# Performance work log

Hardware: AMD Instinct MI355X
Metric: run time of the kernel (lower is better)

## Reference

```python
import jax, jax.numpy as jnp
import numpy as np

NUM_LEVELS = 16
F_PER_LEVEL = 2
LOG2_T = 19
TABLE_SIZE = 1 << LOG2_T  # 524288 entries per level
BASE_RES = 16
DESIRED_RES = 4096
PER_LEVEL_SCALE = np.exp(np.log(DESIRED_RES / BASE_RES) / (NUM_LEVELS - 1))
PRIMES = (np.uint32(1), np.uint32(2654435761), np.uint32(805459861))
N_POINTS = 4_194_304

# 8 corner offsets of the trilinear cell, bit i of corner index -> dim offset
_CORNERS = jnp.array([[(i >> d) & 1 for d in range(3)] for i in range(8)], dtype=jnp.float32)  # [8,3]


def hashgrid_encode(texc, table):
    """texc: [N,3] in [0,1]; table: [L, T, F]. Returns [N, L*F] (tcnn HashGrid math)."""
    feats = []
    for lvl in range(NUM_LEVELS):
        scale = float(np.exp2(lvl * np.log2(PER_LEVEL_SCALE)) * BASE_RES - 1.0)
        res = int(np.ceil(scale)) + 1
        pos = texc * scale + 0.5                    # [N,3]
        pg = jnp.floor(pos)
        frac = pos - pg                             # [N,3]
        corner = pg[:, None, :] + _CORNERS[None]    # [N,8,3]
        ci = corner.astype(jnp.uint32)
        # trilinear weights: prod over dims of frac (offset=1) or 1-frac (offset=0)
        w = jnp.prod(jnp.where(_CORNERS[None] == 1.0, frac[:, None, :], 1.0 - frac[:, None, :]), axis=-1)  # [N,8]
        if res ** 3 <= TABLE_SIZE:
            # dense level: index = x + y*res + z*res^2
            idx = ci[..., 0] + ci[..., 1] * jnp.uint32(res) + ci[..., 2] * jnp.uint32(res * res)
        else:
            # hashed level: spatial hash with xor of per-dim primes, mod 2^19
            idx = (ci[..., 0] * PRIMES[0]) ^ (ci[..., 1] * PRIMES[1]) ^ (ci[..., 2] * PRIMES[2])
            idx = idx & jnp.uint32(TABLE_SIZE - 1)
        g = table[lvl][idx.astype(jnp.int32)]       # [N,8,F] irregular gather
        feats.append(jnp.einsum('nc,ncf->nf', w, g))
    return jnp.concatenate(feats, axis=-1)          # [N, 32]


def setup_inputs() -> dict:
    key = jax.random.key(0)
    k0, k1, k2, k3, k4 = jax.random.split(key, 5)
    texc = jax.random.uniform(k0, (N_POINTS, 3), dtype=jnp.float32)
    # tcnn inits hashgrid params uniform in [-1e-4, 1e-4]
    table = (jax.random.uniform(k1, (NUM_LEVELS, TABLE_SIZE, F_PER_LEVEL), dtype=jnp.float32) * 2.0 - 1.0) * 1e-4
    # kaiming_uniform (relu) bound = sqrt(6/fan_in)
    def kaiming(k, shape):
        bound = float(np.sqrt(6.0 / shape[1]))
        return jax.random.uniform(k, shape, dtype=jnp.float32, minval=-bound, maxval=bound)
    W0 = kaiming(k2, (32, 32))
    W1 = kaiming(k3, (32, 32))
    W2 = kaiming(k4, (3, 32))
    return {"texc": texc, "table": table, "W0": W0, "W1": W1, "W2": W2}


def reference(texc, table, W0, W1, W2):
    enc = hashgrid_encode(texc, table)              # [N,32]
    h = jax.nn.relu(enc @ W0.T)
    h = jax.nn.relu(h @ W1.T)
    out = jax.nn.sigmoid(h @ W2.T)                  # [N,3]
    return out
```

## Files before the change

### kernel.cpp

```cpp
#include <hip/hip_runtime.h>
#include <math.h>

#define NUM_LEVELS 16
#define N_DENSE 5
#define N_HASH (NUM_LEVELS - N_DENSE)
#define TABLE_SIZE (1u << 19)
#define TMASK (TABLE_SIZE - 1u)

typedef float f32x4 __attribute__((ext_vector_type(4)));
typedef float f32x2 __attribute__((ext_vector_type(2)));
typedef short s16x8 __attribute__((ext_vector_type(8)));
typedef unsigned u32x2 __attribute__((ext_vector_type(2)));
typedef unsigned u32x4 __attribute__((ext_vector_type(4)));

struct HashParams { float scale[N_HASH]; };
struct DenseParams { float scale[N_DENSE]; unsigned res[N_DENSE]; };
struct AllParams { float scale[NUM_LEVELS]; unsigned res[NUM_LEVELS]; };

static __device__ __forceinline__ unsigned bf16_bits(float f) {
    const unsigned u = __builtin_bit_cast(unsigned, f);
    return (u + (0x7fffu + ((u >> 16) & 1u))) >> 16;
}
static __device__ __forceinline__ short bf16s(float f) { return (short)bf16_bits(f); }
static __device__ __forceinline__ float bflo(unsigned v) { return __builtin_bit_cast(float, v << 16); }
static __device__ __forceinline__ float bfhi(unsigned v) { return __builtin_bit_cast(float, v & 0xffff0000u); }

static __device__ __forceinline__ s16x8 packW8(const float* __restrict__ p) {
    const f32x4 a = *(const f32x4*)p;
    const f32x4 b = *(const f32x4*)(p + 4);
    s16x8 v;
    v[0] = bf16s(a.x); v[1] = bf16s(a.y); v[2] = bf16s(a.z); v[3] = bf16s(a.w);
    v[4] = bf16s(b.x); v[5] = bf16s(b.y); v[6] = bf16s(b.z); v[7] = bf16s(b.w);
    return v;
}
static __device__ __forceinline__ s16x8 packW8sig(const float* __restrict__ row, int q) {
    const f32x4 lo = *(const f32x4*)(row + 4 * q);
    const f32x4 hi = *(const f32x4*)(row + 16 + 4 * q);
    s16x8 v;
    v[0] = bf16s(lo.x); v[1] = bf16s(hi.x); v[2] = bf16s(lo.y); v[3] = bf16s(hi.y);
    v[4] = bf16s(lo.z); v[5] = bf16s(hi.z); v[6] = bf16s(lo.w); v[7] = bf16s(hi.w);
    return v;
}

__global__ __launch_bounds__(256) void cvt_table_kernel(
    const f32x4* __restrict__ src, u32x2* __restrict__ dst, int n2)
{
    const int i = blockIdx.x * 256 + threadIdx.x;
    if (i >= n2) return;
    const f32x4 g = __builtin_nontemporal_load(src + i);
    u32x2 o;
    o.x = bf16_bits(g.x) | (bf16_bits(g.y) << 16);
    o.y = bf16_bits(g.z) | (bf16_bits(g.w) << 16);
    dst[i] = o;
}

template <bool BT>
__global__ __launch_bounds__(256) void hashed_all_kernel(
    const float* __restrict__ texc,
    const float* __restrict__ tf,
    const unsigned* __restrict__ tb,
    unsigned* __restrict__ enc_ws,
    int n, int B, HashParams P)
{
    __shared__ float tst[768];
    const int tid = threadIdx.x;
    const unsigned lvl = blockIdx.x / (unsigned)B;
    const unsigned blk = blockIdx.x - lvl * (unsigned)B;
    const int i0 = (int)blk * 256;

    tst[tid]       = __builtin_nontemporal_load(texc + 3 * i0 + tid);
    tst[tid + 256] = __builtin_nontemporal_load(texc + 3 * i0 + tid + 256);
    tst[tid + 512] = __builtin_nontemporal_load(texc + 3 * i0 + tid + 512);
    __syncthreads();

    const float s = P.scale[lvl];
    const float tx = tst[3 * tid + 0], ty = tst[3 * tid + 1], tz = tst[3 * tid + 2];

    const float px = tx * s + 0.5f, py = ty * s + 0.5f, pz = tz * s + 0.5f;
    const float gx = floorf(px), gy = floorf(py), gz = floorf(pz);
    const float wx = px - gx, wy = py - gy, wz = pz - gz;
    const unsigned x0 = (unsigned)gx, y0 = (unsigned)gy, z0 = (unsigned)gz;

    const unsigned hy0 = y0 * 2654435761u, hy1 = (y0 + 1u) * 2654435761u;
    const unsigned hz0 = z0 * 805459861u,  hz1 = (z0 + 1u) * 805459861u;
    const unsigned hh[4] = { hy0 ^ hz0, hy1 ^ hz0, hy0 ^ hz1, hy1 ^ hz1 };
    const float wyz[4] = { (1.f - wy) * (1.f - wz), wy * (1.f - wz),
                           (1.f - wy) * wz,         wy * wz };
    const float wx0 = 1.f - wx, wx1 = wx;

    float f0 = 0.f, f1 = 0.f;

    if constexpr (BT) {
        const unsigned* tbl = tb + ((size_t)(N_DENSE + lvl) << 19);
        if ((x0 & 1u) == 0u) {
#pragma unroll
            for (int c = 0; c < 4; ++c) {
                const unsigned idx0 = (x0 ^ hh[c]) & TMASK;
                const u32x2 g = *(const u32x2*)(tbl + (idx0 & ~1u));
                const bool sw = (idx0 & 1u) != 0u;
                const unsigned ea = sw ? g.y : g.x;
                const unsigned eb = sw ? g.x : g.y;
                f0 += wyz[c] * (wx0 * bflo(ea) + wx1 * bflo(eb));
                f1 += wyz[c] * (wx0 * bfhi(ea) + wx1 * bfhi(eb));
            }
        } else {
#pragma unroll
            for (int c = 0; c < 4; ++c) {
                const unsigned ea = tbl[(x0 ^ hh[c]) & TMASK];
                const unsigned eb = tbl[((x0 + 1u) ^ hh[c]) & TMASK];
                f0 += wyz[c] * (wx0 * bflo(ea) + wx1 * bflo(eb));
                f1 += wyz[c] * (wx0 * bfhi(ea) + wx1 * bfhi(eb));
            }
        }
    } else {
        const float* tbl = tf + ((size_t)(N_DENSE + lvl) << 20);
        if ((x0 & 1u) == 0u) {
#pragma unroll
            for (int c = 0; c < 4; ++c) {
                const unsigned idx0 = (x0 ^ hh[c]) & TMASK;
                const f32x4 g = *(const f32x4*)(tbl + 2 * (size_t)(idx0 & ~1u));
                const bool hi = (idx0 & 1u) != 0u;
                const float g0x = hi ? g.z : g.x, g0y = hi ? g.w : g.y;
                const float g1x = hi ? g.x : g.z, g1y = hi ? g.y : g.w;
                f0 += wyz[c] * (wx0 * g0x + wx1 * g1x);
                f1 += wyz[c] * (wx0 * g0y + wx1 * g1y);
            }
        } else {
#pragma unroll
            for (int c = 0; c < 4; ++c) {
                const unsigned ia = (x0 ^ hh[c]) & TMASK;
                const unsigned ib = ((x0 + 1u) ^ hh[c]) & TMASK;
                const f32x2 ga = *(const f32x2*)(tbl + 2 * (size_t)ia);
                const f32x2 gb = *(const f32x2*)(tbl + 2 * (size_t)ib);
                f0 += wyz[c] * (wx0 * ga.x + wx1 * gb.x);
                f1 += wyz[c] * (wx0 * ga.y + wx1 * gb.y);
            }
        }
    }

    const unsigned packed = bf16_bits(f0) | (bf16_bits(f1) << 16);
    __builtin_nontemporal_store(packed, enc_ws + (size_t)lvl * n + (i0 + tid));
}

template <bool BT>
__global__ __launch_bounds__(256) void dense_mlp_kernel(
    const float* __restrict__ texc,
    const float* __restrict__ tf,
    const unsigned* __restrict__ tb,
    const unsigned* __restrict__ enc_ws,
    const float* __restrict__ W0,
    const float* __restrict__ W1,
    const float* __restrict__ W2,
    float* __restrict__ out,
    int n, DenseParams P)
{
    __shared__ float tst[768];
    __shared__ __align__(16) unsigned char slabs[4 * 64 * 80];
    const int tid = threadIdx.x;
    const int i0 = blockIdx.x * 256;

    tst[tid]       = __builtin_nontemporal_load(texc + 3 * i0 + tid);
    tst[tid + 256] = __builtin_nontemporal_load(texc + 3 * i0 + tid + 256);
    tst[tid + 512] = __builtin_nontemporal_load(texc + 3 * i0 + tid + 512);
    __syncthreads();

    const int i = i0 + tid;
    unsigned dd[16];

#pragma unroll
    for (int l = 0; l < N_HASH; ++l)
        dd[N_DENSE + l] = __builtin_nontemporal_load(enc_ws + (size_t)l * n + i);

    const float tx = tst[3 * tid + 0], ty = tst[3 * tid + 1], tz = tst[3 * tid + 2];

#pragma unroll
    for (int l = 0; l < N_DENSE; ++l) {
        const float s = P.scale[l];
        const unsigned res = P.res[l];
        const unsigned res2 = res * res;
        const float px = tx * s + 0.5f, py = ty * s + 0.5f, pz = tz * s + 0.5f;
        const float gx = floorf(px), gy = floorf(py), gz = floorf(pz);
        const float wx = px - gx, wy = py - gy, wz = pz - gz;
        const unsigned x0 = (unsigned)gx, y0 = (unsigned)gy, z0 = (unsigned)gz;
        const float wx0 = 1.f - wx, wx1 = wx;
        const float wyz[4] = { (1.f - wy) * (1.f - wz), wy * (1.f - wz),
                               (1.f - wy) * wz,         wy * wz };
        const unsigned base[4] = { y0 * res + z0 * res2, (y0 + 1u) * res + z0 * res2,
                                   y0 * res + (z0 + 1u) * res2,
                                   (y0 + 1u) * res + (z0 + 1u) * res2 };
        float f0 = 0.f, f1 = 0.f;
        if constexpr (BT) {
            const unsigned* tbl = tb + ((size_t)l << 19);
#pragma unroll
            for (int c = 0; c < 4; ++c) {
                const unsigned idx0 = x0 + base[c];
                unsigned ea, eb;
                if ((idx0 & 1u) == 0u) {
                    const u32x2 g = *(const u32x2*)(tbl + idx0);
                    ea = g.x; eb = g.y;
                } else {
                    ea = tbl[idx0]; eb = tbl[idx0 + 1u];
                }
                f0 += wyz[c] * (wx0 * bflo(ea) + wx1 * bflo(eb));
                f1 += wyz[c] * (wx0 * bfhi(ea) + wx1 * bfhi(eb));
            }
        } else {
            const float* tbl = tf + ((size_t)l << 20);
#pragma unroll
            for (int c = 0; c < 4; ++c) {
                const unsigned idx0 = x0 + base[c];
                if ((idx0 & 1u) == 0u) {
                    const f32x4 g = *(const f32x4*)(tbl + 2 * (size_t)idx0);
                    f0 += wyz[c] * (wx0 * g.x + wx1 * g.z);
                    f1 += wyz[c] * (wx0 * g.y + wx1 * g.w);
                } else {
                    const f32x2 ga = *(const f32x2*)(tbl + 2 * (size_t)idx0);
                    const f32x2 gb = *(const f32x2*)(tbl + 2 * (size_t)(idx0 + 1u));
                    f0 += wyz[c] * (wx0 * ga.x + wx1 * gb.x);
                    f1 += wyz[c] * (wx0 * ga.y + wx1 * gb.y);
                }
            }
        }
        dd[l] = bf16_bits(f0) | (bf16_bits(f1) << 16);
    }

    const int lane = tid & 63;
    const int wv = tid >> 6;
    const int c16 = lane & 15, q = lane >> 4;
    unsigned char* slabB = slabs + wv * (64 * 80);
    unsigned* slab = (unsigned*)slabB;

    *(u32x4*)(slabB + lane * 80 +  0) = (u32x4){ dd[0],  dd[1],  dd[2],  dd[3]  };
    *(u32x4*)(slabB + lane * 80 + 16) = (u32x4){ dd[4],  dd[5],  dd[6],  dd[7]  };
    *(u32x4*)(slabB + lane * 80 + 32) = (u32x4){ dd[8],  dd[9],  dd[10], dd[11] };
    *(u32x4*)(slabB + lane * 80 + 48) = (u32x4){ dd[12], dd[13], dd[14], dd[15] };

    const s16x8 b00 = packW8(W0 + c16 * 32 + 8 * q);
    const s16x8 b01 = packW8(W0 + (16 + c16) * 32 + 8 * q);
    const s16x8 b10 = packW8sig(W1 + c16 * 32, q);
    const s16x8 b11 = packW8sig(W1 + (16 + c16) * 32, q);
    const f32x4 zero4 = { 0.f, 0.f, 0.f, 0.f };

    f32x4 d0[4][2];
#pragma unroll
    for (int t = 0; t < 4; ++t) {
        const s16x8 a = *(const s16x8*)(slabB + (16 * t + c16) * 80 + 16 * q);
        d0[t][0] = __builtin_amdgcn_mfma_f32_16x16x32_bf16(a, b00, zero4, 0, 0, 0);
        d0[t][1] = __builtin_amdgcn_mfma_f32_16x16x32_bf16(a, b01, zero4, 0, 0, 0);
    }
#pragma unroll
    for (int t = 0; t < 4; ++t)
#pragma unroll
        for (int r = 0; r < 4; ++r) {
            const unsigned pk = bf16_bits(fmaxf(d0[t][0][r], 0.f)) |
                                (bf16_bits(fmaxf(d0[t][1][r], 0.f)) << 16);
            slab[(16 * t + 4 * q + r) * 20 + c16] = pk;
        }

    f32x4 d1[4][2];
#pragma unroll
    for (int t = 0; t < 4; ++t) {
        const s16x8 a = *(const s16x8*)(slabB + (16 * t + c16) * 80 + 16 * q);
        d1[t][0] = __builtin_amdgcn_mfma_f32_16x16x32_bf16(a, b10, zero4, 0, 0, 0);
        d1[t][1] = __builtin_amdgcn_mfma_f32_16x16x32_bf16(a, b11, zero4, 0, 0, 0);
    }
#pragma unroll
    for (int t = 0; t < 4; ++t)
#pragma unroll
        for (int r = 0; r < 4; ++r) {
            const unsigned pk = bf16_bits(fmaxf(d1[t][0][r], 0.f)) |
                                (bf16_bits(fmaxf(d1[t][1][r], 0.f)) << 16);
            slab[(16 * t + 4 * q + r) * 20 + c16] = pk;
        }

    float z0 = 0.f, z1 = 0.f, z2 = 0.f;
#pragma unroll
    for (int d = 0; d < 16; ++d) {
        const unsigned v = slab[lane * 20 + d];
        const float a0 = bflo(v), a1 = bfhi(v);
        z0 = fmaf(a0, W2[0 * 32 + d], fmaf(a1, W2[0 * 32 + 16 + d], z0));
        z1 = fmaf(a0, W2[1 * 32 + d], fmaf(a1, W2[1 * 32 + 16 + d], z1));
        z2 = fmaf(a0, W2[2 * 32 + d], fmaf(a1, W2[2 * 32 + 16 + d], z2));
    }
    out[3 * i + 0] = 1.f / (1.f + __expf(-z0));
    out[3 * i + 1] = 1.f / (1.f + __expf(-z1));
    out[3 * i + 2] = 1.f / (1.f + __expf(-z2));
}

__global__ __launch_bounds__(256) void mono_kernel(
    const float* __restrict__ texc, const float* __restrict__ table,
    const float* __restrict__ W0, const float* __restrict__ W1,
    const float* __restrict__ W2, float* __restrict__ out, int n, AllParams p)
{
    int i = blockIdx.x * 256 + threadIdx.x;
    if (i >= n) return;
    const float tx = texc[3 * i], ty = texc[3 * i + 1], tz = texc[3 * i + 2];
    float enc[2 * NUM_LEVELS];
#pragma unroll
    for (int l = 0; l < NUM_LEVELS; ++l) {
        const float s = p.scale[l];
        const unsigned res = p.res[l];
        const float px = tx * s + 0.5f, py = ty * s + 0.5f, pz = tz * s + 0.5f;
        const float gx = floorf(px), gy = floorf(py), gz = floorf(pz);
        const float wx = px - gx, wy = py - gy, wz = pz - gz;
        const unsigned x0 = (unsigned)gx, y0 = (unsigned)gy, z0 = (unsigned)gz;
        const float2* tbl = (const float2*)(table + ((size_t)l << 20));
        float f0 = 0.f, f1 = 0.f;
#pragma unroll
        for (int c = 0; c < 8; ++c) {
            const unsigned dx = c & 1u, dy = (c >> 1) & 1u, dz = (c >> 2) & 1u;
            const unsigned xi = x0 + dx, yi = y0 + dy, zi = z0 + dz;
            unsigned idx;
            if (l < N_DENSE) idx = xi + yi * res + zi * res * res;
            else idx = (xi ^ (yi * 2654435761u) ^ (zi * 805459861u)) & TMASK;
            const float2 g = tbl[idx];
            const float w = (dx ? wx : 1.f - wx) * (dy ? wy : 1.f - wy) *
                            (dz ? wz : 1.f - wz);
            f0 = fmaf(w, g.x, f0);
            f1 = fmaf(w, g.y, f1);
        }
        enc[2 * l] = f0;
        enc[2 * l + 1] = f1;
    }
    float h1[32];
#pragma unroll
    for (int j = 0; j < 32; ++j) {
        float acc = 0.f;
#pragma unroll
        for (int k = 0; k < 32; ++k) acc = fmaf(enc[k], W0[j * 32 + k], acc);
        h1[j] = fmaxf(acc, 0.f);
    }
    float h2[32];
#pragma unroll
    for (int j = 0; j < 32; ++j) {
        float acc = 0.f;
#pragma unroll
        for (int k = 0; k < 32; ++k) acc = fmaf(h1[k], W1[j * 32 + k], acc);
        h2[j] = fmaxf(acc, 0.f);
    }
#pragma unroll
    for (int j = 0; j < 3; ++j) {
        float acc = 0.f;
#pragma unroll
        for (int k = 0; k < 32; ++k) acc = fmaf(h2[k], W2[j * 32 + k], acc);
        out[3 * i + j] = 1.f / (1.f + __expf(-acc));
    }
}

extern "C" void kernel_launch(void* const* d_in, const int* in_sizes, int n_in,
                              void* d_out, int out_size, void* d_ws, size_t ws_size,
                              hipStream_t stream) {
    const float* texc  = (const float*)d_in[0];
    const float* table = (const float*)d_in[1];
    const float* W0    = (const float*)d_in[2];
    const float* W1    = (const float*)d_in[3];
    const float* W2    = (const float*)d_in[4];
    float* out = (float*)d_out;

    const int n = in_sizes[0] / 3;

    AllParams ap;
    const double log2pls = log(4096.0 / 16.0) / 15.0 / log(2.0);
    for (int l = 0; l < NUM_LEVELS; ++l) {
        const double sc = exp2((double)l * log2pls) * 16.0 - 1.0;
        ap.scale[l] = (float)sc;
        ap.res[l] = (unsigned)(ceil(sc) + 1.0);
    }
    HashParams hp;
    for (int l = 0; l < N_HASH; ++l) hp.scale[l] = ap.scale[l + N_DENSE];
    DenseParams dp;
    for (int l = 0; l < N_DENSE; ++l) { dp.scale[l] = ap.scale[l]; dp.res[l] = ap.res[l]; }

    const size_t enc_b = (size_t)N_HASH * (size_t)n * 4u;
    const size_t tbl_b = (size_t)NUM_LEVELS * TABLE_SIZE * 4u;

    if ((n % 256) == 0 && ws_size >= tbl_b + enc_b) {
        unsigned* bt = (unsigned*)d_ws;
        unsigned* enc_ws = bt + (size_t)NUM_LEVELS * TABLE_SIZE;
        const int B = n / 256;
        const int n2 = NUM_LEVELS * TABLE_SIZE / 2;
        cvt_table_kernel<<<(n2 + 255) / 256, 256, 0, stream>>>(
            (const f32x4*)table, (u32x2*)bt, n2);
        hashed_all_kernel<true><<<B * N_HASH, 256, 0, stream>>>(
            texc, table, bt, enc_ws, n, B, hp);
        dense_mlp_kernel<true><<<B, 256, 0, stream>>>(
            texc, table, bt, enc_ws, W0, W1, W2, out, n, dp);
    } else if ((n % 256) == 0 && ws_size >= enc_b) {
        unsigned* enc_ws = (unsigned*)d_ws;
        const int B = n / 256;
        hashed_all_kernel<false><<<B * N_HASH, 256, 0, stream>>>(
            texc, table, nullptr, enc_ws, n, B, hp);
        dense_mlp_kernel<false><<<B, 256, 0, stream>>>(
            texc, table, nullptr, enc_ws, W0, W1, W2, out, n, dp);
    } else {
        const int blocks = (n + 255) / 256;
        mono_kernel<<<blocks, 256, 0, stream>>>(texc, table, W0, W1, W2, out, n, ap);
    }
}
```

Measured before the change: 1.282 ms.

## Move first two hashed levels into the dense+MLP kernel

Computes the two lowest-resolution hashed levels directly inside the dense/MLP kernel instead of in the separate hashed kernel. This removes the workspace write and read of their encodings and shrinks the hashed kernel grid. In exchange the dense kernel gets more gather work and register pressure, which may reduce its occupancy or lengthen its critical path.

```diff
diff --git a/kernel.cpp b/kernel.cpp
--- a/kernel.cpp
+++ b/kernel.cpp
@@ -4,6 +4,8 @@
 #define NUM_LEVELS 16
 #define N_DENSE 5
 #define N_HASH (NUM_LEVELS - N_DENSE)
+#define N_MOVED 2
+#define N_HASH_OUT (N_HASH - N_MOVED)
 #define TABLE_SIZE (1u << 19)
 #define TMASK (TABLE_SIZE - 1u)
 
@@ -13,8 +15,8 @@
 typedef unsigned u32x2 __attribute__((ext_vector_type(2)));
 typedef unsigned u32x4 __attribute__((ext_vector_type(4)));
 
-struct HashParams { float scale[N_HASH]; };
-struct DenseParams { float scale[N_DENSE]; unsigned res[N_DENSE]; };
+struct HashParams { float scale[N_HASH_OUT]; };
+struct DenseParams { float scale[N_DENSE]; unsigned res[N_DENSE]; float hscale[N_MOVED]; };
 struct AllParams { float scale[NUM_LEVELS]; unsigned res[NUM_LEVELS]; };
 
 static __device__ __forceinline__ unsigned bf16_bits(float f) {
@@ -91,7 +93,7 @@
     float f0 = 0.f, f1 = 0.f;
 
     if constexpr (BT) {
-        const unsigned* tbl = tb + ((size_t)(N_DENSE + lvl) << 19);
+        const unsigned* tbl = tb + ((size_t)(N_DENSE + N_MOVED + lvl) << 19);
         if ((x0 & 1u) == 0u) {
 #pragma unroll
             for (int c = 0; c < 4; ++c) {
@@ -113,7 +115,7 @@
             }
         }
     } else {
-        const float* tbl = tf + ((size_t)(N_DENSE + lvl) << 20);
+        const float* tbl = tf + ((size_t)(N_DENSE + N_MOVED + lvl) << 20);
         if ((x0 & 1u) == 0u) {
 #pragma unroll
             for (int c = 0; c < 4; ++c) {
@@ -168,8 +170,8 @@
     unsigned dd[16];
 
 #pragma unroll
-    for (int l = 0; l < N_HASH; ++l)
-        dd[N_DENSE + l] = __builtin_nontemporal_load(enc_ws + (size_t)l * n + i);
+    for (int l = 0; l < N_HASH_OUT; ++l)
+        dd[N_DENSE + N_MOVED + l] = __builtin_nontemporal_load(enc_ws + (size_t)l * n + i);
 
     const float tx = tst[3 * tid + 0], ty = tst[3 * tid + 1], tz = tst[3 * tid + 2];
 
@@ -224,6 +226,72 @@
         dd[l] = bf16_bits(f0) | (bf16_bits(f1) << 16);
     }
 
+#pragma unroll
+    for (int m = 0; m < N_MOVED; ++m) {
+        const float s = P.hscale[m];
+        const float px = tx * s + 0.5f, py = ty * s + 0.5f, pz = tz * s + 0.5f;
+        const float gx = floorf(px), gy = floorf(py), gz = floorf(pz);
+        const float wx = px - gx, wy = py - gy, wz = pz - gz;
+        const unsigned x0 = (unsigned)gx, y0 = (unsigned)gy, z0 = (unsigned)gz;
+
+        const unsigned hy0 = y0 * 2654435761u, hy1 = (y0 + 1u) * 2654435761u;
+        const unsigned hz0 = z0 * 805459861u,  hz1 = (z0 + 1u) * 805459861u;
+        const unsigned hh[4] = { hy0 ^ hz0, hy1 ^ hz0, hy0 ^ hz1, hy1 ^ hz1 };
+        const float wyz[4] = { (1.f - wy) * (1.f - wz), wy * (1.f - wz),
+                               (1.f - wy) * wz,         wy * wz };
+        const float wx0 = 1.f - wx, wx1 = wx;
+
+        float f0 = 0.f, f1 = 0.f;
+        if constexpr (BT) {
+            const unsigned* tbl = tb + ((size_t)(N_DENSE + m) << 19);
+            if ((x0 & 1u) == 0u) {
+#pragma unroll
+                for (int c = 0; c < 4; ++c) {
+                    const unsigned idx0 = (x0 ^ hh[c]) & TMASK;
+                    const u32x2 g = *(const u32x2*)(tbl + (idx0 & ~1u));
+                    const bool sw = (idx0 & 1u) != 0u;
+                    const unsigned ea = sw ? g.y : g.x;
+                    const unsigned eb = sw ? g.x : g.y;
+                    f0 += wyz[c] * (wx0 * bflo(ea) + wx1 * bflo(eb));
+                    f1 += wyz[c] * (wx0 * bfhi(ea) + wx1 * bfhi(eb));
+                }
+            } else {
+#pragma unroll
+                for (int c = 0; c < 4; ++c) {
+                    const unsigned ea = tbl[(x0 ^ hh[c]) & TMASK];
+                    const unsigned eb = tbl[((x0 + 1u) ^ hh[c]) & TMASK];
+                    f0 += wyz[c] * (wx0 * bflo(ea) + wx1 * bflo(eb));
+                    f1 += wyz[c] * (wx0 * bfhi(ea) + wx1 * bfhi(eb));
+                }
+            }
+        } else {
+            const float* tbl = tf + ((size_t)(N_DENSE + m) << 20);
+            if ((x0 & 1u) == 0u) {
+#pragma unroll
+                for (int c = 0; c < 4; ++c) {
+                    const unsigned idx0 = (x0 ^ hh[c]) & TMASK;
+                    const f32x4 g = *(const f32x4*)(tbl + 2 * (size_t)(idx0 & ~1u));
+                    const bool hi = (idx0 & 1u) != 0u;
+                    const float g0x = hi ? g.z : g.x, g0y = hi ? g.w : g.y;
+                    const float g1x = hi ? g.x : g.z, g1y = hi ? g.y : g.w;
+                    f0 += wyz[c] * (wx0 * g0x + wx1 * g1x);
+                    f1 += wyz[c] * (wx0 * g0y + wx1 * g1y);
+                }
+            } else {
+#pragma unroll
+                for (int c = 0; c < 4; ++c) {
+                    const unsigned ia = (x0 ^ hh[c]) & TMASK;
+                    const unsigned ib = ((x0 + 1u) ^ hh[c]) & TMASK;
+                    const f32x2 ga = *(const f32x2*)(tbl + 2 * (size_t)ia);
+                    const f32x2 gb = *(const f32x2*)(tbl + 2 * (size_t)ib);
+                    f0 += wyz[c] * (wx0 * ga.x + wx1 * gb.x);
+                    f1 += wyz[c] * (wx0 * ga.y + wx1 * gb.y);
+                }
+            }
+        }
+        dd[N_DENSE + m] = bf16_bits(f0) | (bf16_bits(f1) << 16);
+    }
+
     const int lane = tid & 63;
     const int wv = tid >> 6;
     const int c16 = lane & 15, q = lane >> 4;
@@ -367,11 +435,12 @@
         ap.res[l] = (unsigned)(ceil(sc) + 1.0);
     }
     HashParams hp;
-    for (int l = 0; l < N_HASH; ++l) hp.scale[l] = ap.scale[l + N_DENSE];
+    for (int l = 0; l < N_HASH_OUT; ++l) hp.scale[l] = ap.scale[l + N_DENSE + N_MOVED];
     DenseParams dp;
     for (int l = 0; l < N_DENSE; ++l) { dp.scale[l] = ap.scale[l]; dp.res[l] = ap.res[l]; }
-
-    const size_t enc_b = (size_t)N_HASH * (size_t)n * 4u;
+    for (int m = 0; m < N_MOVED; ++m) dp.hscale[m] = ap.scale[N_DENSE + m];
+
+    const size_t enc_b = (size_t)N_HASH_OUT * (size_t)n * 4u;
     const size_t tbl_b = (size_t)NUM_LEVELS * TABLE_SIZE * 4u;
 
     if ((n % 256) == 0 && ws_size >= tbl_b + enc_b) {
@@ -381,14 +450,14 @@
         const int n2 = NUM_LEVELS * TABLE_SIZE / 2;
         cvt_table_kernel<<<(n2 + 255) / 256, 256, 0, stream>>>(
             (const f32x4*)table, (u32x2*)bt, n2);
-        hashed_all_kernel<true><<<B * N_HASH, 256, 0, stream>>>(
+        hashed_all_kernel<true><<<B * N_HASH_OUT, 256, 0, stream>>>(
             texc, table, bt, enc_ws, n, B, hp);
         dense_mlp_kernel<true><<<B, 256, 0, stream>>>(
             texc, table, bt, enc_ws, W0, W1, W2, out, n, dp);
     } else if ((n % 256) == 0 && ws_size >= enc_b) {
         unsigned* enc_ws = (unsigned*)d_ws;
         const int B = n / 256;
-        hashed_all_kernel<false><<<B * N_HASH, 256, 0, stream>>>(
+        hashed_all_kernel<false><<<B * N_HASH_OUT, 256, 0, stream>>>(
             texc, table, nullptr, enc_ws, n, B, hp);
         dense_mlp_kernel<false><<<B, 256, 0, stream>>>(
             texc, table, nullptr, enc_ws, W0, W1, W2, out, n, dp);
```

Result: slower. 1.401 ms (+9.3%).

## Add permuted bf16 table copy so odd-aligned corner pairs load as one 8-byte read

Applied to the files above, without the earlier changes.

The table conversion kernel now also writes a second bf16 table whose four-entry groups are permuted as (0,3,1,2). That places entries 1-2 (and, swapped, 3-0) adjacent and 8-byte aligned. In both the hashed and dense kernels, odd-x corner pairs that previously needed two scalar 4-byte gathers can now read one aligned 8-byte element from this copy. The cost is an extra table write in the conversion pass, more workspace, and a larger footprint competing for cache. The second fallback path is rewritten oddly: it converts the table twice into the same buffer and then runs the fp32 path.

```diff
diff --git a/kernel.cpp b/kernel.cpp
--- a/kernel.cpp
+++ b/kernel.cpp
@@ -43,22 +43,27 @@
 }
 
 __global__ __launch_bounds__(256) void cvt_table_kernel(
-    const f32x4* __restrict__ src, u32x2* __restrict__ dst, int n2)
+    const f32x4* __restrict__ src, u32x4* __restrict__ bt4,
+    u32x4* __restrict__ p34, int n4)
 {
     const int i = blockIdx.x * 256 + threadIdx.x;
-    if (i >= n2) return;
-    const f32x4 g = __builtin_nontemporal_load(src + i);
-    u32x2 o;
-    o.x = bf16_bits(g.x) | (bf16_bits(g.y) << 16);
-    o.y = bf16_bits(g.z) | (bf16_bits(g.w) << 16);
-    dst[i] = o;
-}
-
-template <bool BT>
+    if (i >= n4) return;
+    const f32x4 a = __builtin_nontemporal_load(src + 2 * (size_t)i);
+    const f32x4 b = __builtin_nontemporal_load(src + 2 * (size_t)i + 1);
+    const unsigned pk0 = bf16_bits(a.x) | (bf16_bits(a.y) << 16);
+    const unsigned pk1 = bf16_bits(a.z) | (bf16_bits(a.w) << 16);
+    const unsigned pk2 = bf16_bits(b.x) | (bf16_bits(b.y) << 16);
+    const unsigned pk3 = bf16_bits(b.z) | (bf16_bits(b.w) << 16);
+    __builtin_nontemporal_store((u32x4){ pk0, pk1, pk2, pk3 }, bt4 + i);
+    __builtin_nontemporal_store((u32x4){ pk0, pk3, pk1, pk2 }, p34 + i);
+}
+
+template <int MODE>
 __global__ __launch_bounds__(256) void hashed_all_kernel(
     const float* __restrict__ texc,
     const float* __restrict__ tf,
     const unsigned* __restrict__ tb,
+    const u32x2* __restrict__ p3,
     unsigned* __restrict__ enc_ws,
     int n, int B, HashParams P)
 {
@@ -90,7 +95,7 @@
 
     float f0 = 0.f, f1 = 0.f;
 
-    if constexpr (BT) {
+    if constexpr (MODE >= 1) {
         const unsigned* tbl = tb + ((size_t)(N_DENSE + lvl) << 19);
         if ((x0 & 1u) == 0u) {
 #pragma unroll
@@ -103,6 +108,20 @@
                 f0 += wyz[c] * (wx0 * bflo(ea) + wx1 * bflo(eb));
                 f1 += wyz[c] * (wx0 * bfhi(ea) + wx1 * bfhi(eb));
             }
+        } else if (MODE == 2 && (x0 & 2u) == 0u) {
+            const u32x2* p3l = p3 + ((size_t)(N_DENSE + lvl) << 18);
+#pragma unroll
+            for (int c = 0; c < 4; ++c) {
+                const unsigned a = (x0 ^ hh[c]) & TMASK;
+                const bool sw = (a & 2u) != 0u;
+                const unsigned jj = sw ? (a ^ 3u) : a;
+                const unsigned sc = ((jj >> 2) << 1) | (jj & 1u);
+                const u32x2 g = p3l[sc];
+                const unsigned ea = sw ? g.y : g.x;
+                const unsigned eb = sw ? g.x : g.y;
+                f0 += wyz[c] * (wx0 * bflo(ea) + wx1 * bflo(eb));
+                f1 += wyz[c] * (wx0 * bfhi(ea) + wx1 * bfhi(eb));
+            }
         } else {
 #pragma unroll
             for (int c = 0; c < 4; ++c) {
@@ -130,8 +149,8 @@
             for (int c = 0; c < 4; ++c) {
                 const unsigned ia = (x0 ^ hh[c]) & TMASK;
                 const unsigned ib = ((x0 + 1u) ^ hh[c]) & TMASK;
-                const f32x2 ga = *(const f32x2*)(tbl + 2 * (size_t)ia);
-                const f32x2 gb = *(const f32x2*)(tbl + 2 * (size_t)ib);
+                const f32x2 ga = *(const f32x2*)(tf + ((size_t)(N_DENSE + lvl) << 20) + 2 * (size_t)ia);
+                const f32x2 gb = *(const f32x2*)(tf + ((size_t)(N_DENSE + lvl) << 20) + 2 * (size_t)ib);
                 f0 += wyz[c] * (wx0 * ga.x + wx1 * gb.x);
                 f1 += wyz[c] * (wx0 * ga.y + wx1 * gb.y);
             }
@@ -142,11 +161,12 @@
     __builtin_nontemporal_store(packed, enc_ws + (size_t)lvl * n + (i0 + tid));
 }
 
-template <bool BT>
+template <int MODE>
 __global__ __launch_bounds__(256) void dense_mlp_kernel(
     const float* __restrict__ texc,
     const float* __restrict__ tf,
     const unsigned* __restrict__ tb,
+    const u32x2* __restrict__ p3,
     const unsigned* __restrict__ enc_ws,
     const float* __restrict__ W0,
     const float* __restrict__ W1,
@@ -189,14 +209,18 @@
                                    y0 * res + (z0 + 1u) * res2,
                                    (y0 + 1u) * res + (z0 + 1u) * res2 };
         float f0 = 0.f, f1 = 0.f;
-        if constexpr (BT) {
+        if constexpr (MODE >= 1) {
             const unsigned* tbl = tb + ((size_t)l << 19);
+            const u32x2* p3l = p3 + ((size_t)l << 18);
 #pragma unroll
             for (int c = 0; c < 4; ++c) {
                 const unsigned idx0 = x0 + base[c];
                 unsigned ea, eb;
                 if ((idx0 & 1u) == 0u) {
                     const u32x2 g = *(const u32x2*)(tbl + idx0);
+                    ea = g.x; eb = g.y;
+                } else if (MODE == 2 && (idx0 & 2u) == 0u) {
+                    const u32x2 g = p3l[((idx0 >> 2) << 1) | 1u];
                     ea = g.x; eb = g.y;
                 } else {
                     ea = tbl[idx0]; eb = tbl[idx0 + 1u];
@@ -373,25 +397,45 @@
 
     const size_t enc_b = (size_t)N_HASH * (size_t)n * 4u;
     const size_t tbl_b = (size_t)NUM_LEVELS * TABLE_SIZE * 4u;
-
-    if ((n % 256) == 0 && ws_size >= tbl_b + enc_b) {
+    const size_t p3_b  = (size_t)NUM_LEVELS * (TABLE_SIZE / 2) * 8u;
+
+    if ((n % 256) == 0 && ws_size >= tbl_b + p3_b + enc_b) {
+        unsigned* bt = (unsigned*)d_ws;
+        u32x2* p3 = (u32x2*)(bt + (size_t)NUM_LEVELS * TABLE_SIZE);
+        unsigned* enc_ws = (unsigned*)(p3 + (size_t)NUM_LEVELS * (TABLE_SIZE / 2));
+        const int B = n / 256;
+        const int n4 = NUM_LEVELS * TABLE_SIZE / 4;
+        cvt_table_kernel<<<(n4 + 255) / 256, 256, 0, stream>>>(
+            (const f32x4*)table, (u32x4*)bt, (u32x4*)p3, n4);
+        hashed_all_kernel<2><<<B * N_HASH, 256, 0, stream>>>(
+            texc, table, bt, p3, enc_ws, n, B, hp);
+        dense_mlp_kernel<2><<<B, 256, 0, stream>>>(
+            texc, table, bt, p3, enc_ws, W0, W1, W2, out, n, dp);
+    } else if ((n % 256) == 0 && ws_size >= tbl_b + enc_b) {
         unsigned* bt = (unsigned*)d_ws;
         unsigned* enc_ws = bt + (size_t)NUM_LEVELS * TABLE_SIZE;
         const int B = n / 256;
-        const int n2 = NUM_LEVELS * TABLE_SIZE / 2;
-        cvt_table_kernel<<<(n2 + 255) / 256, 256, 0, stream>>>(
-            (const f32x4*)table, (u32x2*)bt, n2);
-        hashed_all_kernel<true><<<B * N_HASH, 256, 0, stream>>>(
-            texc, table, bt, enc_ws, n, B, hp);
-        dense_mlp_kernel<true><<<B, 256, 0, stream>>>(
-            texc, table, bt, enc_ws, W0, W1, W2, out, n, dp);
+        const int n4 = NUM_LEVELS * TABLE_SIZE / 4;
+        {
+            struct Local {
+                static __host__ void dummy() {}
+            };
+            cvt_table_kernel<<<(n4 + 255) / 256, 256, 0, stream>>>(
+                (const f32x4*)table, (u32x4*)bt, (u32x4*)bt, n4);
+            cvt_table_kernel<<<(n4 + 255) / 256, 256, 0, stream>>>(
+                (const f32x4*)table, (u32x4*)bt, (u32x4*)bt, n4);
+        }
+        hashed_all_kernel<0><<<B * N_HASH, 256, 0, stream>>>(
+            texc, table, nullptr, nullptr, enc_ws, n, B, hp);
+        dense_mlp_kernel<0><<<B, 256, 0, stream>>>(
+            texc, table, nullptr, nullptr, enc_ws, W0, W1, W2, out, n, dp);
     } else if ((n % 256) == 0 && ws_size >= enc_b) {
         unsigned* enc_ws = (unsigned*)d_ws;
         const int B = n / 256;
-        hashed_all_kernel<false><<<B * N_HASH, 256, 0, stream>>>(
-            texc, table, nullptr, enc_ws, n, B, hp);
-        dense_mlp_kernel<false><<<B, 256, 0, stream>>>(
-            texc, table, nullptr, enc_ws, W0, W1, W2, out, n, dp);
+        hashed_all_kernel<0><<<B * N_HASH, 256, 0, stream>>>(
+            texc, table, nullptr, nullptr, enc_ws, n, B, hp);
+        dense_mlp_kernel<0><<<B, 256, 0, stream>>>(
+            texc, table, nullptr, nullptr, enc_ws, W0, W1, W2, out, n, dp);
     } else {
         const int blocks = (n + 255) / 256;
         mono_kernel<<<blocks, 256, 0, stream>>>(texc, table, W0, W1, W2, out, n, ap);
```

Result: slower. 1.422 ms (+10.9%).
